# Optimization experiments

Measured on AMD Instinct MI355X. Metric: run time of the kernel, lower is better.

## Reference

```python
import jax, jax.numpy as jnp
import numpy as np

N, D, C = 4096, 2048, 128
MARGIN = 0.3


def _choice(key, mask):
    # Uniform random choice among True entries of mask (Gumbel-max trick).
    g = jax.random.gumbel(key, mask.shape, jnp.float32)
    return jnp.argmax(jnp.where(mask, g, -jnp.inf))


def setup_inputs() -> dict:
    key = jax.random.key(0)
    k1, k2, k3, k4, k5 = jax.random.split(key, 5)
    return {
        "inputs": jax.random.normal(k1, (N, D), jnp.float32),
        "prediction": jax.random.normal(k2, (N, C), jnp.float32),
        "targets": jax.random.randint(k3, (N,), 0, C),
        "true_targets": jax.random.randint(k4, (N,), 0, C),
        "prob": jax.random.uniform(k5, (N,), jnp.float32),
        "threshold": jnp.float32(0.5),
    }


def _forward(inputs, prediction, prob, threshold, targets, true_targets):
    n = inputs.shape[0]
    # Pairwise Euclidean distances: ||xi||^2 + ||xj||^2 - 2 xi.xj  (clamped, sqrt)
    sq = jnp.sum(inputs * inputs, axis=1)
    dist = jnp.sqrt(jnp.clip(sq[:, None] + sq[None, :] - 2.0 * (inputs @ inputs.T), 1e-12, None))
    is_pos = targets[:, None] == targets[None, :]
    confident = prob >= threshold
    pred_cls = jnp.argmax(prediction, axis=1)

    # 12 closest negatives per row (rank 0 = hardest; ranks 1..11 cover the
    # original's fallback loop of at most 10 extra steps, j in 1..11).
    neg_dist = jnp.where(is_pos, jnp.inf, dist)
    _, neg_rank = jax.lax.top_k(-neg_dist, 12)  # [n, 12] indices

    row_keys = jax.random.split(jax.random.key(42), n)
    idx = jnp.arange(n)

    def per_row(i, rk):
        di = dist[i]
        pos_mask = is_pos[i]
        kp, kr = jax.random.split(rk)
        rp = _choice(kp, pos_mask & (idx != i))  # random positive != anchor
        hn = neg_rank[i, 0]                      # hardest negative
        ap0, an0 = di[rp], di[hn]
        p_pos = prob[rp] >= threshold
        p_neg = prob[hn] >= threshold
        is_FN = pred_cls[hn] == targets[i]

        # Case B (pos confident, neg unconfident, false-negative):
        # first confident negative among ranks 1..11, else rank 11.
        cand = neg_rank[i, 1:12]
        conf_c = prob[cand] >= threshold
        hn_new = cand[jnp.where(jnp.any(conf_c), jnp.argmax(conf_c), 10)]
        apB, anB = (ap0 + an0) * 0.5, di[hn_new]

        # Cases C / D-not-FN: resample positive, up to 6 draws total,
        # first draw that is confident and != anchor, else the last draw.
        draws = jax.vmap(lambda k: _choice(k, pos_mask))(jax.random.split(kr, 6))
        valid = (draws != i) & (prob[draws] >= threshold)
        rp_new = draws[jnp.where(jnp.any(valid), jnp.argmax(valid), 5)]
        apC, anC = di[rp_new], (ap0 + an0) * 0.5

        useB = p_pos & ~p_neg & is_FN
        useC = (~p_pos & p_neg) | (~p_pos & ~p_neg & ~is_FN)
        inverse = ~p_pos & ~p_neg & is_FN  # keep ap0/an0, flip hinge direction

        ap = jnp.where(useB, apB, jnp.where(useC, apC, ap0))
        an = jnp.where(useB, anB, jnp.where(useC, anC, an0))
        per_loss = jnp.where(inverse,
                             jnp.maximum(an - ap + MARGIN, 0.0),
                             jnp.maximum(ap - an + MARGIN, 0.0))
        return ap, an, per_loss

    aps, ans, losses = jax.vmap(per_row)(idx, row_keys)
    cnt = jnp.sum(confident)
    loss_sum = jnp.sum(jnp.where(confident, losses, 0.0))
    loss = jnp.where(cnt > 0, loss_sum / jnp.maximum(cnt, 1).astype(loss_sum.dtype),
                     jnp.zeros((), loss_sum.dtype))
    correct = jnp.sum(confident & (ans >= aps))
    return loss, correct, cnt


def reference(inputs, prediction, targets, true_targets, prob, threshold):
    return _forward(inputs, prediction, prob, threshold, targets, true_targets)
```

## Files before the change

### kernel.cpp

```cpp
#include <hip/hip_runtime.h>
#include <hip/hip_bf16.h>
#include <cstdint>
#include <cmath>

#define NROWS 4096
#define DIM   2048
#define CNUM  128
#define MARGIN_F 0.3f
#define TOPK 12
#define MAXM 256
#define GBK 32
#define CAP 160

#define BM 64
#define BN 64
#define BK 16
#define SLICES 8
#define COLS_PER_SLICE (NROWS / SLICES)

typedef _Float16 f16x8 __attribute__((ext_vector_type(8)));
typedef float    f32x4 __attribute__((ext_vector_type(4)));

#define GLD_LDS16(g, l)                                                        \
    __builtin_amdgcn_global_load_lds(                                          \
        (const __attribute__((address_space(1))) uint32_t*)(g),                \
        (__attribute__((address_space(3))) uint32_t*)(l), 16, 0, 0)

__device__ __forceinline__ uint32_t rnd_u32(uint32_t row, uint32_t k) {
    uint64_t x = ((uint64_t)row << 32) ^ (0x9E3779B97F4A7C15ULL * (uint64_t)(k + 1u));
    x ^= x >> 33; x *= 0xff51afd7ed558ccdULL;
    x ^= x >> 33; x *= 0xc4ceb9fe1a85ec53ULL;
    x ^= x >> 33;
    return (uint32_t)x;
}

__global__ void rowsq_kernel(const float* __restrict__ X, float* __restrict__ sq) {
    int wave = (blockIdx.x * blockDim.x + threadIdx.x) >> 6;
    int lane = threadIdx.x & 63;
    if (wave >= NROWS) return;
    const float4* xp = (const float4*)(X + (size_t)wave * DIM);
    float s = 0.f;
    for (int k = lane; k < DIM / 4; k += 64) {
        float4 v = xp[k];
        s += v.x * v.x + v.y * v.y + v.z * v.z + v.w * v.w;
    }
    for (int off = 32; off; off >>= 1) s += __shfl_xor(s, off, 64);
    if (lane == 0) sq[wave] = s;
}

__global__ void prep_kernel(const float* __restrict__ X, _Float16* __restrict__ Xh,
                            float* __restrict__ sq) {
    __shared__ float ws[4];
    int row = blockIdx.x, tid = threadIdx.x;
    int wave = tid >> 6, lane = tid & 63;
    const float4* xp = (const float4*)(X + (size_t)row * DIM);
    float4 a = xp[tid * 2], b = xp[tid * 2 + 1];
    float s = a.x * a.x + a.y * a.y + a.z * a.z + a.w * a.w
            + b.x * b.x + b.y * b.y + b.z * b.z + b.w * b.w;
    _Float16 h[8] = { (_Float16)a.x, (_Float16)a.y, (_Float16)a.z, (_Float16)a.w,
                      (_Float16)b.x, (_Float16)b.y, (_Float16)b.z, (_Float16)b.w };
    ((uint4*)(Xh + (size_t)row * DIM))[tid] = *(uint4*)h;
    for (int off = 32; off; off >>= 1) s += __shfl_xor(s, off, 64);
    if (lane == 0) ws[wave] = s;
    __syncthreads();
    if (tid == 0) sq[row] = ws[0] + ws[1] + ws[2] + ws[3];
}

__global__ void predcls_kernel(const float* __restrict__ P, int* __restrict__ cls) {
    int row = (blockIdx.x * blockDim.x + threadIdx.x) >> 6;
    int lane = threadIdx.x & 63;
    if (row >= NROWS) return;
    const float* p = P + (size_t)row * CNUM;
    float v0 = p[lane]; int i0 = lane;
    float v1 = p[lane + 64];
    if (v1 > v0) { v0 = v1; i0 = lane + 64; }
    for (int off = 1; off < 64; off <<= 1) {
        float ov = __shfl_xor(v0, off, 64);
        int   oi = __shfl_xor(i0, off, 64);
        if (ov > v0 || (ov == v0 && oi < i0)) { v0 = ov; i0 = oi; }
    }
    if (lane == 0) cls[row] = i0;
}

__global__ void classlist_kernel(const int* __restrict__ tgt,
                                 int* __restrict__ cnt, int* __restrict__ members) {
    int c = (blockIdx.x * blockDim.x + threadIdx.x) >> 6;
    int lane = threadIdx.x & 63;
    if (c >= CNUM) return;
    int k = 0;
    for (int base = 0; base < NROWS; base += 64) {
        int i = base + lane;
        bool m = (tgt[i] == c);
        unsigned long long mask = __ballot(m);
        if (m) {
            int pos = k + __popcll(mask & ((1ull << lane) - 1ull));
            if (pos < MAXM) members[c * MAXM + pos] = i;
        }
        k += __popcll(mask);
    }
    if (lane == 0) cnt[c] = (k < MAXM) ? k : MAXM;
}

__launch_bounds__(256, 4)
__global__ void mfma_dist_kernel(const _Float16* __restrict__ Xh,
                                 const float* __restrict__ sq, const int* __restrict__ tgt,
                                 _Float16* __restrict__ dist) {
    __shared__ _Float16 Ah[2][128 * GBK];
    __shared__ _Float16 Bh[2][128 * GBK];
    __shared__ float    trb[4][16 * 17];
    __shared__ float    sqA[128], sqB[128];
    __shared__ int      tgA[128], tgB[128];

    int b = blockIdx.x;
    int br = 0, S = 0;
    while (b >= S + (32 - br)) { S += 32 - br; br++; }
    int bc = br + (b - S);

    int r0 = br * 128, c0 = bc * 128;
    int tid = threadIdx.x;
    int wave = tid >> 6, lane = tid & 63;
    int wr = wave >> 1, wc = wave & 1;

    if (tid < 128) { sqA[tid] = sq[r0 + tid]; tgA[tid] = tgt[r0 + tid]; }
    else { int t = tid - 128; sqB[t] = sq[c0 + t]; tgB[t] = tgt[c0 + t]; }

    f32x4 acc[4][4];
#pragma unroll
    for (int i = 0; i < 4; i++)
#pragma unroll
        for (int j = 0; j < 4; j++) acc[i][j] = (f32x4)0.f;

    const _Float16* gA[2]; const _Float16* gB[2];
    int ldsOff[2];
#pragma unroll
    for (int q = 0; q < 2; q++) {
        int rl = wave * 32 + q * 16 + (lane >> 2);
        int slot = lane & 3;
        int c = (slot - ((rl >> 1) & 3)) & 3;
        gA[q] = Xh + (size_t)(r0 + rl) * DIM + c * 8;
        gB[q] = Xh + (size_t)(c0 + rl) * DIM + c * 8;
        ldsOff[q] = (wave * 32 + q * 16) * GBK;
    }

    auto stage = [&](int buf, int kOff) {
#pragma unroll
        for (int q = 0; q < 2; q++) {
            GLD_LDS16(gA[q] + kOff, &Ah[buf][ldsOff[q]]);
            GLD_LDS16(gB[q] + kOff, &Bh[buf][ldsOff[q]]);
        }
    };

    stage(0, 0);
    int fr = lane & 15, fq = lane >> 4;

    for (int it = 0; it < DIM / GBK; it++) {
        int cur = it & 1;
        __syncthreads();
        if (it + 1 < DIM / GBK) stage(cur ^ 1, (it + 1) * GBK);
        f16x8 af[4], bf[4];
#pragma unroll
        for (int i = 0; i < 4; i++) {
            int row = wr * 64 + i * 16 + fr;
            int slot = (fq + ((row >> 1) & 3)) & 3;
            af[i] = *(const f16x8*)&Ah[cur][row * GBK + slot * 8];
        }
#pragma unroll
        for (int j = 0; j < 4; j++) {
            int col = wc * 64 + j * 16 + fr;
            int slot = (fq + ((col >> 1) & 3)) & 3;
            bf[j] = *(const f16x8*)&Bh[cur][col * GBK + slot * 8];
        }
#pragma unroll
        for (int i = 0; i < 4; i++)
#pragma unroll
            for (int j = 0; j < 4; j++)
                acc[i][j] = __builtin_amdgcn_mfma_f32_16x16x32_f16(af[i], bf[j], acc[i][j], 0, 0, 0);
    }

    float* tb = trb[wave];
#pragma unroll
    for (int i = 0; i < 4; i++) {
#pragma unroll
        for (int j = 0; j < 4; j++) {
            int lcol = wc * 64 + j * 16 + fr;
            float d[4];
#pragma unroll
            for (int r = 0; r < 4; r++) {
                int lrow = wr * 64 + i * 16 + fq * 4 + r;
                float v = sqA[lrow] + sqB[lcol] - 2.f * acc[i][j][r];
                if (tgA[lrow] == tgB[lcol]) v = INFINITY;
                d[r] = v;
                __builtin_nontemporal_store((_Float16)v,
                    &dist[(size_t)(r0 + lrow) * NROWS + (c0 + lcol)]);
            }
            if (br != bc) {
#pragma unroll
                for (int r = 0; r < 4; r++) tb[fr * 17 + fq * 4 + r] = d[r];
#pragma unroll
                for (int r = 0; r < 4; r++) {
                    float v = tb[(fq * 4 + r) * 17 + fr];
                    int grow = c0 + wc * 64 + j * 16 + fq * 4 + r;
                    int gcol = r0 + wr * 64 + i * 16 + fr;
                    __builtin_nontemporal_store((_Float16)v,
                        &dist[(size_t)grow * NROWS + gcol]);
                }
            }
        }
    }
}

__launch_bounds__(256)
__global__ void topk_kernel(const _Float16* __restrict__ dist,
                            float* __restrict__ top_v, int* __restrict__ top_i) {
    __shared__ float cbv[4][CAP];
    __shared__ int   cbi[4][CAP];
    int wave = threadIdx.x >> 6, lane = threadIdx.x & 63;
    int row = blockIdx.x * 4 + wave;
    const f16x8* d = (const f16x8*)(dist + (size_t)row * NROWS);

    f16x8 v[8];
#pragma unroll
    for (int t = 0; t < 8; t++) v[t] = d[t * 64 + lane];

    float lmin = INFINITY, lmax = -INFINITY, lsum = 0.f;
    int lcnt = 0;
#pragma unroll
    for (int t = 0; t < 8; t++) {
#pragma unroll
        for (int c = 0; c < 8; c++) {
            float x = (float)v[t][c];
            bool fin = x < INFINITY;
            lmin = fminf(lmin, x);
            lmax = fmaxf(lmax, fin ? x : -INFINITY);
            lsum += fin ? x : 0.f;
            lcnt += fin ? 1 : 0;
        }
    }
    for (int off = 32; off; off >>= 1) {
        lmin = fminf(lmin, __shfl_xor(lmin, off, 64));
        lmax = fmaxf(lmax, __shfl_xor(lmax, off, 64));
        lsum += __shfl_xor(lsum, off, 64);
        lcnt += __shfl_xor(lcnt, off, 64);
    }
    float mu = lsum / (float)(lcnt > 0 ? lcnt : 1);

    float lo = lmin, hi = lmax + 1.0f;
    float tau = lmin + 0.3f * (mu - lmin);
    if (!(tau > lo && tau < hi)) tau = 0.5f * (lo + hi);
    for (int it = 0; it < 32; it++) {
        int lc = 0;
#pragma unroll
        for (int t = 0; t < 8; t++) {
#pragma unroll
            for (int c = 0; c < 8; c++) lc += ((float)v[t][c] < tau) ? 1 : 0;
        }
        for (int off = 32; off; off >>= 1) lc += __shfl_xor(lc, off, 64);
        if (lc >= TOPK && lc <= CAP) break;
        if (lc < TOPK) lo = tau; else hi = tau;
        tau = 0.5f * (lo + hi);
    }

    int cnt = 0;
#pragma unroll
    for (int t = 0; t < 8; t++) {
#pragma unroll
        for (int c = 0; c < 8; c++) {
            float x = (float)v[t][c];
            bool p = x < tau;
            unsigned long long mk = __ballot(p);
            if (p) {
                int pos = cnt + __popcll(mk & ((1ull << lane) - 1ull));
                if (pos < CAP) {
                    cbv[wave][pos] = x;
                    cbi[wave][pos] = (t * 64 + lane) * 8 + c;
                }
            }
            cnt += __popcll(mk);
        }
    }
    if (cnt > CAP) cnt = CAP;

    float mv[3]; int mi[3];
#pragma unroll
    for (int r = 0; r < 3; r++) {
        int p = r * 64 + lane;
        bool ok = p < cnt;
        mv[r] = ok ? cbv[wave][p] : INFINITY;
        mi[r] = ok ? cbi[wave][p] : 0x7FFFFFFF;
    }

    for (int t = 0; t < TOPK; t++) {
        float bv = mv[0]; int bi = mi[0];
        if (mv[1] < bv || (mv[1] == bv && mi[1] < bi)) { bv = mv[1]; bi = mi[1]; }
        if (mv[2] < bv || (mv[2] == bv && mi[2] < bi)) { bv = mv[2]; bi = mi[2]; }
        for (int off = 32; off; off >>= 1) {
            float ov = __shfl_xor(bv, off, 64);
            int   oi = __shfl_xor(bi, off, 64);
            if (ov < bv || (ov == bv && oi < bi)) { bv = ov; bi = oi; }
        }
        if (lane == 0) {
            top_v[(size_t)row * TOPK + t] = bv;
            int si = (bi >= 0 && bi < NROWS) ? bi : 0;
            top_i[(size_t)row * TOPK + t] = si;
        }
#pragma unroll
        for (int r = 0; r < 3; r++)
            if (mi[r] == bi) { mv[r] = INFINITY; mi[r] = 0x7FFFFFFF; }
    }
}

__launch_bounds__(256)
__global__ void dist_topk_kernel(const float* __restrict__ X, const float* __restrict__ sq,
                                 const int* __restrict__ tgt,
                                 float* __restrict__ part_v, int* __restrict__ part_i) {
    __shared__ float As[BK][BM];
    __shared__ float Bs[BK][BN];
    __shared__ float Cs[BM][BN + 1];
    __shared__ float sqA[BM], sqB[BN];
    __shared__ int   tgA[BM], tgB[BN];

    int rowBase = blockIdx.x * BM;
    int slice = blockIdx.y;
    int tid = threadIdx.x;
    int tx = tid & 15, ty = tid >> 4;

    if (tid < BM) { sqA[tid] = sq[rowBase + tid]; tgA[tid] = tgt[rowBase + tid]; }

    float lv[TOPK]; int li[TOPK];
#pragma unroll
    for (int k = 0; k < TOPK; k++) { lv[k] = INFINITY; li[k] = -1; }

    for (int jt = 0; jt < COLS_PER_SLICE / BN; jt++) {
        int colBase = slice * COLS_PER_SLICE + jt * BN;
        __syncthreads();
        if (tid < BN) { sqB[tid] = sq[colBase + tid]; tgB[tid] = tgt[colBase + tid]; }

        float acc[4][4] = {};
        for (int kb = 0; kb < DIM; kb += BK) {
            int r  = tid >> 2;
            int kk = (tid & 3) * 4;
            float4 va = *(const float4*)(X + (size_t)(rowBase + r) * DIM + kb + kk);
            As[kk + 0][r] = va.x; As[kk + 1][r] = va.y; As[kk + 2][r] = va.z; As[kk + 3][r] = va.w;
            float4 vb = *(const float4*)(X + (size_t)(colBase + r) * DIM + kb + kk);
            Bs[kk + 0][r] = vb.x; Bs[kk + 1][r] = vb.y; Bs[kk + 2][r] = vb.z; Bs[kk + 3][r] = vb.w;
            __syncthreads();
#pragma unroll
            for (int k = 0; k < BK; k++) {
                float a[4], b2[4];
                *(float4*)a = *(const float4*)&As[k][ty * 4];
                *(float4*)b2 = *(const float4*)&Bs[k][tx * 4];
#pragma unroll
                for (int i2 = 0; i2 < 4; i2++)
#pragma unroll
                    for (int j2 = 0; j2 < 4; j2++)
                        acc[i2][j2] += a[i2] * b2[j2];
            }
            __syncthreads();
        }
#pragma unroll
        for (int i2 = 0; i2 < 4; i2++) {
            int r = ty * 4 + i2;
#pragma unroll
            for (int j2 = 0; j2 < 4; j2++) {
                int c = tx * 4 + j2;
                float d2 = sqA[r] + sqB[c] - 2.f * acc[i2][j2];
                if (tgA[r] == tgB[c]) d2 = INFINITY;
                Cs[r][c] = d2;
            }
        }
        __syncthreads();
        if (tid < BM) {
            int r = tid;
            for (int c = 0; c < BN; c++) {
                float v = Cs[r][c];
                if (v < lv[TOPK - 1]) {
                    float nv = v; int ni = colBase + c;
#pragma unroll
                    for (int p = 0; p < TOPK; p++) {
                        if (nv < lv[p]) {
                            float tv = lv[p]; int ti = li[p];
                            lv[p] = nv; li[p] = ni;
                            nv = tv; ni = ti;
                        }
                    }
                }
            }
        }
    }
    if (tid < BM) {
        int r = tid;
#pragma unroll
        for (int k = 0; k < TOPK; k++) {
            size_t o = ((size_t)(rowBase + r) * SLICES + slice) * TOPK + k;
            part_v[o] = lv[k];
            part_i[o] = li[k];
        }
    }
}

__global__ void topk_merge_kernel(const float* __restrict__ part_v, const int* __restrict__ part_i,
                                  float* __restrict__ top_v, int* __restrict__ top_i) {
    int row = blockIdx.x * blockDim.x + threadIdx.x;
    if (row >= NROWS) return;
    float lv[TOPK]; int li[TOPK];
#pragma unroll
    for (int k = 0; k < TOPK; k++) { lv[k] = INFINITY; li[k] = -1; }
    for (int s = 0; s < SLICES; s++) {
        for (int k = 0; k < TOPK; k++) {
            size_t o = ((size_t)row * SLICES + s) * TOPK + k;
            float v = part_v[o];
            if (!(v < lv[TOPK - 1])) break;
            int idx = part_i[o];
            float nv = v; int ni = idx;
#pragma unroll
            for (int p = 0; p < TOPK; p++) {
                if (nv < lv[p]) {
                    float tv = lv[p]; int ti = li[p];
                    lv[p] = nv; li[p] = ni;
                    nv = tv; ni = ti;
                }
            }
        }
    }
#pragma unroll
    for (int k = 0; k < TOPK; k++) {
        top_v[(size_t)row * TOPK + k] = lv[k];
        top_i[(size_t)row * TOPK + k] = li[k];
    }
}

__global__ void rowlogic_kernel(const _Float16* __restrict__ Xh, const float* __restrict__ sq,
                                const float* __restrict__ prob, const float* __restrict__ thr_p,
                                const int* __restrict__ tgt, const int* __restrict__ pred_cls,
                                const int* __restrict__ class_cnt, const int* __restrict__ class_mem,
                                const float* __restrict__ top_v, const int* __restrict__ top_i,
                                float* __restrict__ row_loss, int* __restrict__ row_corr) {
    int i = (blockIdx.x * blockDim.x + threadIdx.x) >> 6;
    int lane = threadIdx.x & 63;
    if (i >= NROWS) return;
    float thr = *thr_p;

    int c = tgt[i];
    int cc = class_cnt[c];
    const int* mem = class_mem + c * MAXM;

    int pos_i = 0;
    for (int k = 0; k < cc; k++) { if (mem[k] == i) { pos_i = k; break; } }

    int rp = 0;
    if (cc > 1) {
        uint32_t r = rnd_u32((uint32_t)i, 0x9111u) % (uint32_t)(cc - 1);
        if ((int)r >= pos_i) r++;
        rp = mem[r];
    }

    int hn = top_i[(size_t)i * TOPK + 0];
    float an0 = sqrtf(fmaxf(top_v[(size_t)i * TOPK + 0], 1e-12f));
    bool p_neg = prob[hn] >= thr;
    bool is_FN = (pred_cls[hn] == c);

    int sel = 11;
    for (int k = 1; k <= 11; k++) {
        int cd = top_i[(size_t)i * TOPK + k];
        if (prob[cd] >= thr) { sel = k; break; }
    }
    float anB = sqrtf(fmaxf(top_v[(size_t)i * TOPK + sel], 1e-12f));

    int first_valid = -1, last_draw = 0;
    for (int k = 0; k < 6; k++) {
        uint32_t r = rnd_u32((uint32_t)i, 0xD000u + (uint32_t)k) % (uint32_t)(cc > 0 ? cc : 1);
        int dk = mem[r];
        last_draw = dk;
        if (first_valid < 0 && dk != i && prob[dk] >= thr) first_valid = dk;
    }
    int rp_new = (first_valid >= 0) ? first_valid : last_draw;
    bool p_pos = prob[rp] >= thr;

    const f16x8* xi = (const f16x8*)(Xh + (size_t)i * DIM);
    const f16x8* xr = (const f16x8*)(Xh + (size_t)rp * DIM);
    const f16x8* xn = (const f16x8*)(Xh + (size_t)rp_new * DIM);
    float s1 = 0.f, s2 = 0.f;
    for (int k = lane; k < DIM / 8; k += 64) {
        f16x8 a = xi[k], b = xr[k], d = xn[k];
#pragma unroll
        for (int e = 0; e < 8; e++) {
            float ax = (float)a[e];
            s1 += ax * (float)b[e];
            s2 += ax * (float)d[e];
        }
    }
    for (int off = 32; off; off >>= 1) {
        s1 += __shfl_xor(s1, off, 64);
        s2 += __shfl_xor(s2, off, 64);
    }
    if (lane == 0) {
        float ap0 = sqrtf(fmaxf(sq[i] + sq[rp]     - 2.f * s1, 1e-12f));
        float apC = sqrtf(fmaxf(sq[i] + sq[rp_new] - 2.f * s2, 1e-12f));
        float apB = (ap0 + an0) * 0.5f;
        float anC = (ap0 + an0) * 0.5f;
        bool useB = p_pos && !p_neg && is_FN;
        bool useC = (!p_pos && p_neg) || (!p_pos && !p_neg && !is_FN);
        bool inverse = !p_pos && !p_neg && is_FN;
        float ap = useB ? apB : (useC ? apC : ap0);
        float an = useB ? anB : (useC ? anC : an0);
        float pl = inverse ? fmaxf(an - ap + MARGIN_F, 0.f)
                           : fmaxf(ap - an + MARGIN_F, 0.f);
        bool conf = prob[i] >= thr;
        row_loss[i] = conf ? pl : 0.f;
        row_corr[i] = (conf && (an >= ap)) ? 1 : 0;
    }
}

__global__ void rowlogic_f32_kernel(const float* __restrict__ X, const float* __restrict__ sq,
                                    const float* __restrict__ prob, const float* __restrict__ thr_p,
                                    const int* __restrict__ tgt, const int* __restrict__ pred_cls,
                                    const int* __restrict__ class_cnt, const int* __restrict__ class_mem,
                                    const float* __restrict__ top_v, const int* __restrict__ top_i,
                                    float* __restrict__ row_loss, int* __restrict__ row_corr) {
    int i = (blockIdx.x * blockDim.x + threadIdx.x) >> 6;
    int lane = threadIdx.x & 63;
    if (i >= NROWS) return;
    float thr = *thr_p;

    int c = tgt[i];
    int cc = class_cnt[c];
    const int* mem = class_mem + c * MAXM;

    int pos_i = 0;
    for (int k = 0; k < cc; k++) { if (mem[k] == i) { pos_i = k; break; } }

    int rp = 0;
    if (cc > 1) {
        uint32_t r = rnd_u32((uint32_t)i, 0x9111u) % (uint32_t)(cc - 1);
        if ((int)r >= pos_i) r++;
        rp = mem[r];
    }

    int hn = top_i[(size_t)i * TOPK + 0];
    float an0 = sqrtf(fmaxf(top_v[(size_t)i * TOPK + 0], 1e-12f));
    bool p_neg = prob[hn] >= thr;
    bool is_FN = (pred_cls[hn] == c);

    int sel = 11;
    for (int k = 1; k <= 11; k++) {
        int cd = top_i[(size_t)i * TOPK + k];
        if (prob[cd] >= thr) { sel = k; break; }
    }
    float anB = sqrtf(fmaxf(top_v[(size_t)i * TOPK + sel], 1e-12f));

    int first_valid = -1, last_draw = 0;
    for (int k = 0; k < 6; k++) {
        uint32_t r = rnd_u32((uint32_t)i, 0xD000u + (uint32_t)k) % (uint32_t)(cc > 0 ? cc : 1);
        int dk = mem[r];
        last_draw = dk;
        if (first_valid < 0 && dk != i && prob[dk] >= thr) first_valid = dk;
    }
    int rp_new = (first_valid >= 0) ? first_valid : last_draw;
    bool p_pos = prob[rp] >= thr;

    const float4* xi = (const float4*)(X + (size_t)i * DIM);
    const float4* xr = (const float4*)(X + (size_t)rp * DIM);
    const float4* xn = (const float4*)(X + (size_t)rp_new * DIM);
    float s1 = 0.f, s2 = 0.f;
    for (int k = lane; k < DIM / 4; k += 64) {
        float4 a = xi[k], b = xr[k], d = xn[k];
        s1 += a.x * b.x + a.y * b.y + a.z * b.z + a.w * b.w;
        s2 += a.x * d.x + a.y * d.y + a.z * d.z + a.w * d.w;
    }
    for (int off = 32; off; off >>= 1) {
        s1 += __shfl_xor(s1, off, 64);
        s2 += __shfl_xor(s2, off, 64);
    }
    if (lane == 0) {
        float ap0 = sqrtf(fmaxf(sq[i] + sq[rp]     - 2.f * s1, 1e-12f));
        float apC = sqrtf(fmaxf(sq[i] + sq[rp_new] - 2.f * s2, 1e-12f));
        float apB = (ap0 + an0) * 0.5f;
        float anC = (ap0 + an0) * 0.5f;
        bool useB = p_pos && !p_neg && is_FN;
        bool useC = (!p_pos && p_neg) || (!p_pos && !p_neg && !is_FN);
        bool inverse = !p_pos && !p_neg && is_FN;
        float ap = useB ? apB : (useC ? apC : ap0);
        float an = useB ? anB : (useC ? anC : an0);
        float pl = inverse ? fmaxf(an - ap + MARGIN_F, 0.f)
                           : fmaxf(ap - an + MARGIN_F, 0.f);
        bool conf = prob[i] >= thr;
        row_loss[i] = conf ? pl : 0.f;
        row_corr[i] = (conf && (an >= ap)) ? 1 : 0;
    }
}

__global__ void reduce_kernel(const float* __restrict__ row_loss, const int* __restrict__ row_corr,
                              const float* __restrict__ prob, const float* __restrict__ thr_p,
                              float* __restrict__ out) {
    __shared__ float sl[256];
    __shared__ int   sc[256];
    __shared__ int   sn[256];
    float thr = *thr_p;
    int tid = threadIdx.x;
    float l = 0.f; int corr = 0, cnt = 0;
    for (int i = tid; i < NROWS; i += 256) {
        l += row_loss[i];
        corr += row_corr[i];
        cnt += (prob[i] >= thr) ? 1 : 0;
    }
    sl[tid] = l; sc[tid] = corr; sn[tid] = cnt;
    __syncthreads();
    for (int off = 128; off; off >>= 1) {
        if (tid < off) {
            sl[tid] += sl[tid + off];
            sc[tid] += sc[tid + off];
            sn[tid] += sn[tid + off];
        }
        __syncthreads();
    }
    if (tid == 0) {
        int cn = sn[0];
        float loss = (cn > 0) ? (sl[0] / (float)(cn > 1 ? cn : 1)) : 0.f;
        out[0] = loss;
        out[1] = (float)sc[0];
        out[2] = (float)cn;
    }
}

extern "C" void kernel_launch(void* const* d_in, const int* in_sizes, int n_in,
                              void* d_out, int out_size, void* d_ws, size_t ws_size,
                              hipStream_t stream) {
    const float* X    = (const float*)d_in[0];
    const float* P    = (const float*)d_in[1];
    const int*   tgt  = (const int*)d_in[2];
    const float* prob = (const float*)d_in[4];
    const float* thr  = (const float*)d_in[5];
    float* out = (float*)d_out;

    char* w = (char*)d_ws;
    auto alloc = [&](size_t bytes) {
        char* p = w;
        w += (bytes + 255) & ~(size_t)255;
        return p;
    };
    float* sq        = (float*)alloc(NROWS * sizeof(float));
    int*   pred_cls  = (int*)  alloc(NROWS * sizeof(int));
    int*   class_cnt = (int*)  alloc(CNUM * sizeof(int));
    int*   class_mem = (int*)  alloc((size_t)CNUM * MAXM * sizeof(int));
    float* top_v     = (float*)alloc((size_t)NROWS * TOPK * sizeof(float));
    int*   top_i     = (int*)  alloc((size_t)NROWS * TOPK * sizeof(int));
    float* row_loss  = (float*)alloc(NROWS * sizeof(float));
    int*   row_corr  = (int*)  alloc(NROWS * sizeof(int));
    char*  var_base  = w;

    size_t fast_need = (size_t)NROWS * DIM * 2 + (size_t)NROWS * NROWS * 2 + (1 << 20);
    bool fast = ((size_t)(var_base - (char*)d_ws) + fast_need) <= ws_size;

    predcls_kernel<<<NROWS / 4, 256, 0, stream>>>(P, pred_cls);
    classlist_kernel<<<CNUM / 4, 256, 0, stream>>>(tgt, class_cnt, class_mem);

    if (fast) {
        _Float16* Xh   = (_Float16*)alloc((size_t)NROWS * DIM * 2);
        _Float16* dist = (_Float16*)alloc((size_t)NROWS * NROWS * 2);
        prep_kernel<<<NROWS, 256, 0, stream>>>(X, Xh, sq);
        mfma_dist_kernel<<<528, 256, 0, stream>>>(Xh, sq, tgt, dist);
        topk_kernel<<<NROWS / 4, 256, 0, stream>>>(dist, top_v, top_i);
        rowlogic_kernel<<<NROWS / 4, 256, 0, stream>>>(Xh, sq, prob, thr, tgt, pred_cls,
                                                       class_cnt, class_mem, top_v, top_i,
                                                       row_loss, row_corr);
    } else {
        rowsq_kernel<<<NROWS / 4, 256, 0, stream>>>(X, sq);
        float* part_v = (float*)alloc((size_t)NROWS * SLICES * TOPK * sizeof(float));
        int*   part_i = (int*)  alloc((size_t)NROWS * SLICES * TOPK * sizeof(int));
        dist_topk_kernel<<<dim3(NROWS / BM, SLICES), 256, 0, stream>>>(X, sq, tgt, part_v, part_i);
        topk_merge_kernel<<<NROWS / 256, 256, 0, stream>>>(part_v, part_i, top_v, top_i);
        rowlogic_f32_kernel<<<NROWS / 4, 256, 0, stream>>>(X, sq, prob, thr, tgt, pred_cls,
                                                           class_cnt, class_mem, top_v, top_i,
                                                           row_loss, row_corr);
    }

    reduce_kernel<<<1, 256, 0, stream>>>(row_loss, row_corr, prob, thr, out);
}
```

Measured before the change: 240.1 us.

## Fuse setup kernels and store distance matrix in fp32

Merges the prep, predicted-class, and class-list kernels into one launch to cut launch overhead. It also switches the intermediate distance matrix from fp16 to fp32 and uses nontemporal loads in top-k. This doubles the distance matrix traffic (64MB instead of 32MB) and the workspace requirement, which could make the fast path fall back if the workspace is too small. In exchange it avoids fp16 rounding and overflow in the stored distances.

```diff
diff --git a/kernel.cpp b/kernel.cpp
--- a/kernel.cpp
+++ b/kernel.cpp
@@ -32,6 +32,58 @@
     x ^= x >> 33; x *= 0xc4ceb9fe1a85ec53ULL;
     x ^= x >> 33;
     return (uint32_t)x;
+}
+
+__global__ void setup_kernel(const float* __restrict__ X, _Float16* __restrict__ Xh,
+                             float* __restrict__ sq,
+                             const float* __restrict__ P, int* __restrict__ cls,
+                             const int* __restrict__ tgt,
+                             int* __restrict__ cnt, int* __restrict__ members) {
+    int b = blockIdx.x, tid = threadIdx.x;
+    int wave = tid >> 6, lane = tid & 63;
+
+    if (b < NROWS) {
+        __shared__ float ws[4];
+        int row = b;
+        const float4* xp = (const float4*)(X + (size_t)row * DIM);
+        float4 a = xp[tid * 2], v2 = xp[tid * 2 + 1];
+        float s = a.x * a.x + a.y * a.y + a.z * a.z + a.w * a.w
+                + v2.x * v2.x + v2.y * v2.y + v2.z * v2.z + v2.w * v2.w;
+        _Float16 h[8] = { (_Float16)a.x, (_Float16)a.y, (_Float16)a.z, (_Float16)a.w,
+                          (_Float16)v2.x, (_Float16)v2.y, (_Float16)v2.z, (_Float16)v2.w };
+        ((uint4*)(Xh + (size_t)row * DIM))[tid] = *(uint4*)h;
+        for (int off = 32; off; off >>= 1) s += __shfl_xor(s, off, 64);
+        if (lane == 0) ws[wave] = s;
+        __syncthreads();
+        if (tid == 0) sq[row] = ws[0] + ws[1] + ws[2] + ws[3];
+    } else if (b < NROWS + NROWS / 4) {
+        int row = (b - NROWS) * 4 + wave;
+        const float* p = P + (size_t)row * CNUM;
+        float v0 = p[lane]; int i0 = lane;
+        float v1 = p[lane + 64];
+        if (v1 > v0) { v0 = v1; i0 = lane + 64; }
+        for (int off = 1; off < 64; off <<= 1) {
+            float ov = __shfl_xor(v0, off, 64);
+            int   oi = __shfl_xor(i0, off, 64);
+            if (ov > v0 || (ov == v0 && oi < i0)) { v0 = ov; i0 = oi; }
+        }
+        if (lane == 0) cls[row] = i0;
+    } else {
+        int c = (b - NROWS - NROWS / 4) * 4 + wave;
+        if (c >= CNUM) return;
+        int k = 0;
+        for (int base = 0; base < NROWS; base += 64) {
+            int i = base + lane;
+            bool m = (tgt[i] == c);
+            unsigned long long mask = __ballot(m);
+            if (m) {
+                int pos = k + __popcll(mask & ((1ull << lane) - 1ull));
+                if (pos < MAXM) members[c * MAXM + pos] = i;
+            }
+            k += __popcll(mask);
+        }
+        if (lane == 0) cnt[c] = (k < MAXM) ? k : MAXM;
+    }
 }
 
 __global__ void rowsq_kernel(const float* __restrict__ X, float* __restrict__ sq) {
@@ -46,24 +98,6 @@
     }
     for (int off = 32; off; off >>= 1) s += __shfl_xor(s, off, 64);
     if (lane == 0) sq[wave] = s;
-}
-
-__global__ void prep_kernel(const float* __restrict__ X, _Float16* __restrict__ Xh,
-                            float* __restrict__ sq) {
-    __shared__ float ws[4];
-    int row = blockIdx.x, tid = threadIdx.x;
-    int wave = tid >> 6, lane = tid & 63;
-    const float4* xp = (const float4*)(X + (size_t)row * DIM);
-    float4 a = xp[tid * 2], b = xp[tid * 2 + 1];
-    float s = a.x * a.x + a.y * a.y + a.z * a.z + a.w * a.w
-            + b.x * b.x + b.y * b.y + b.z * b.z + b.w * b.w;
-    _Float16 h[8] = { (_Float16)a.x, (_Float16)a.y, (_Float16)a.z, (_Float16)a.w,
-                      (_Float16)b.x, (_Float16)b.y, (_Float16)b.z, (_Float16)b.w };
-    ((uint4*)(Xh + (size_t)row * DIM))[tid] = *(uint4*)h;
-    for (int off = 32; off; off >>= 1) s += __shfl_xor(s, off, 64);
-    if (lane == 0) ws[wave] = s;
-    __syncthreads();
-    if (tid == 0) sq[row] = ws[0] + ws[1] + ws[2] + ws[3];
 }
 
 __global__ void predcls_kernel(const float* __restrict__ P, int* __restrict__ cls) {
@@ -104,7 +138,7 @@
 __launch_bounds__(256, 4)
 __global__ void mfma_dist_kernel(const _Float16* __restrict__ Xh,
                                  const float* __restrict__ sq, const int* __restrict__ tgt,
-                                 _Float16* __restrict__ dist) {
+                                 float* __restrict__ dist) {
     __shared__ _Float16 Ah[2][128 * GBK];
     __shared__ _Float16 Bh[2][128 * GBK];
     __shared__ float    trb[4][16 * 17];
@@ -190,8 +224,7 @@
                 float v = sqA[lrow] + sqB[lcol] - 2.f * acc[i][j][r];
                 if (tgA[lrow] == tgB[lcol]) v = INFINITY;
                 d[r] = v;
-                __builtin_nontemporal_store((_Float16)v,
-                    &dist[(size_t)(r0 + lrow) * NROWS + (c0 + lcol)]);
+                __builtin_nontemporal_store(v, &dist[(size_t)(r0 + lrow) * NROWS + (c0 + lcol)]);
             }
             if (br != bc) {
 #pragma unroll
@@ -201,8 +234,7 @@
                     float v = tb[(fq * 4 + r) * 17 + fr];
                     int grow = c0 + wc * 64 + j * 16 + fq * 4 + r;
                     int gcol = r0 + wr * 64 + i * 16 + fr;
-                    __builtin_nontemporal_store((_Float16)v,
-                        &dist[(size_t)grow * NROWS + gcol]);
+                    __builtin_nontemporal_store(v, &dist[(size_t)grow * NROWS + gcol]);
                 }
             }
         }
@@ -210,25 +242,25 @@
 }
 
 __launch_bounds__(256)
-__global__ void topk_kernel(const _Float16* __restrict__ dist,
+__global__ void topk_kernel(const float* __restrict__ dist,
                             float* __restrict__ top_v, int* __restrict__ top_i) {
     __shared__ float cbv[4][CAP];
     __shared__ int   cbi[4][CAP];
     int wave = threadIdx.x >> 6, lane = threadIdx.x & 63;
     int row = blockIdx.x * 4 + wave;
-    const f16x8* d = (const f16x8*)(dist + (size_t)row * NROWS);
-
-    f16x8 v[8];
-#pragma unroll
-    for (int t = 0; t < 8; t++) v[t] = d[t * 64 + lane];
+    const f32x4* d = (const f32x4*)(dist + (size_t)row * NROWS);
+
+    f32x4 v[16];
+#pragma unroll
+    for (int t = 0; t < 16; t++) v[t] = __builtin_nontemporal_load(&d[t * 64 + lane]);
 
     float lmin = INFINITY, lmax = -INFINITY, lsum = 0.f;
     int lcnt = 0;
 #pragma unroll
-    for (int t = 0; t < 8; t++) {
-#pragma unroll
-        for (int c = 0; c < 8; c++) {
-            float x = (float)v[t][c];
+    for (int t = 0; t < 16; t++) {
+#pragma unroll
+        for (int c = 0; c < 4; c++) {
+            float x = v[t][c];
             bool fin = x < INFINITY;
             lmin = fminf(lmin, x);
             lmax = fmaxf(lmax, fin ? x : -INFINITY);
@@ -250,9 +282,8 @@
     for (int it = 0; it < 32; it++) {
         int lc = 0;
 #pragma unroll
-        for (int t = 0; t < 8; t++) {
-#pragma unroll
-            for (int c = 0; c < 8; c++) lc += ((float)v[t][c] < tau) ? 1 : 0;
+        for (int t = 0; t < 16; t++) {
+            lc += (v[t][0] < tau) + (v[t][1] < tau) + (v[t][2] < tau) + (v[t][3] < tau);
         }
         for (int off = 32; off; off >>= 1) lc += __shfl_xor(lc, off, 64);
         if (lc >= TOPK && lc <= CAP) break;
@@ -262,17 +293,17 @@
 
     int cnt = 0;
 #pragma unroll
-    for (int t = 0; t < 8; t++) {
-#pragma unroll
-        for (int c = 0; c < 8; c++) {
-            float x = (float)v[t][c];
+    for (int t = 0; t < 16; t++) {
+#pragma unroll
+        for (int c = 0; c < 4; c++) {
+            float x = v[t][c];
             bool p = x < tau;
             unsigned long long mk = __ballot(p);
             if (p) {
                 int pos = cnt + __popcll(mk & ((1ull << lane) - 1ull));
                 if (pos < CAP) {
                     cbv[wave][pos] = x;
-                    cbi[wave][pos] = (t * 64 + lane) * 8 + c;
+                    cbi[wave][pos] = (t * 64 + lane) * 4 + c;
                 }
             }
             cnt += __popcll(mk);
@@ -648,16 +679,14 @@
     int*   row_corr  = (int*)  alloc(NROWS * sizeof(int));
     char*  var_base  = w;
 
-    size_t fast_need = (size_t)NROWS * DIM * 2 + (size_t)NROWS * NROWS * 2 + (1 << 20);
+    size_t fast_need = (size_t)NROWS * DIM * 2 + (size_t)NROWS * NROWS * 4 + (1 << 20);
     bool fast = ((size_t)(var_base - (char*)d_ws) + fast_need) <= ws_size;
-
-    predcls_kernel<<<NROWS / 4, 256, 0, stream>>>(P, pred_cls);
-    classlist_kernel<<<CNUM / 4, 256, 0, stream>>>(tgt, class_cnt, class_mem);
 
     if (fast) {
         _Float16* Xh   = (_Float16*)alloc((size_t)NROWS * DIM * 2);
-        _Float16* dist = (_Float16*)alloc((size_t)NROWS * NROWS * 2);
-        prep_kernel<<<NROWS, 256, 0, stream>>>(X, Xh, sq);
+        float*    dist = (float*)alloc((size_t)NROWS * NROWS * 4);
+        setup_kernel<<<NROWS + NROWS / 4 + CNUM / 4, 256, 0, stream>>>(
+            X, Xh, sq, P, pred_cls, tgt, class_cnt, class_mem);
         mfma_dist_kernel<<<528, 256, 0, stream>>>(Xh, sq, tgt, dist);
         topk_kernel<<<NROWS / 4, 256, 0, stream>>>(dist, top_v, top_i);
         rowlogic_kernel<<<NROWS / 4, 256, 0, stream>>>(Xh, sq, prob, thr, tgt, pred_cls,
@@ -665,6 +694,8 @@
                                                        row_loss, row_corr);
     } else {
         rowsq_kernel<<<NROWS / 4, 256, 0, stream>>>(X, sq);
+        predcls_kernel<<<NROWS / 4, 256, 0, stream>>>(P, pred_cls);
+        classlist_kernel<<<CNUM / 4, 256, 0, stream>>>(tgt, class_cnt, class_mem);
         float* part_v = (float*)alloc((size_t)NROWS * SLICES * TOPK * sizeof(float));
         int*   part_i = (int*)  alloc((size_t)NROWS * SLICES * TOPK * sizeof(int));
         dist_topk_kernel<<<dim3(NROWS / BM, SLICES), 256, 0, stream>>>(X, sq, tgt, part_v, part_i);
```

After: 222.7 us. -7.2%, faster.
